# Kernel tuning notes

Hardware: AMD Instinct MI355X
Metric: run time of the kernel (lower is better)

## Reference

```python
import jax, jax.numpy as jnp
import numpy as np

RADIUS = 0.8
NSAMPLE = 32
EPS = 1e-5  # BatchNorm eps


def _bn(x, gamma, beta, axes):
    # BatchNorm (training-mode batch statistics), channel dim kept via broadcasting
    m = jnp.mean(x, axis=axes, keepdims=True)
    v = jnp.var(x, axis=axes, keepdims=True)
    return (x - m) * jax.lax.rsqrt(v + EPS) * gamma + beta


def setup_inputs() -> dict:
    key = jax.random.key(0)
    ks = jax.random.split(key, 6)
    B, N, P, C, COUT = 4, 8192, 2048, 128, 256
    ffps_xyz = jax.random.uniform(ks[0], (B, P, 3), dtype=jnp.float32) * 2.0 - 1.0
    backbone_xyz = jax.random.uniform(ks[1], (B, N, 3), dtype=jnp.float32) * 2.0 - 1.0
    backbone_features = jax.random.normal(ks[2], (B, C, N), dtype=jnp.float32)
    w_shift = jax.random.normal(ks[3], (3, 3), dtype=jnp.float32) * 0.1
    gamma_shift = jnp.ones((3,), jnp.float32)
    beta_shift = jnp.zeros((3,), jnp.float32)
    w_mlp = jax.random.normal(ks[4], (COUT, 3 + C), dtype=jnp.float32) * 0.05
    gamma_mlp = jnp.ones((COUT,), jnp.float32)
    beta_mlp = jnp.zeros((COUT,), jnp.float32)
    return {
        "ffps_xyz": ffps_xyz,
        "backbone_xyz": backbone_xyz,
        "backbone_features": backbone_features,
        "w_shift": w_shift,
        "gamma_shift": gamma_shift,
        "beta_shift": beta_shift,
        "w_mlp": w_mlp,
        "gamma_mlp": gamma_mlp,
        "beta_mlp": beta_mlp,
    }


def reference(ffps_xyz, backbone_xyz, backbone_features,
              w_shift, gamma_shift, beta_shift,
              w_mlp, gamma_mlp, beta_mlp):
    B, P, _ = ffps_xyz.shape
    N = backbone_xyz.shape[1]

    # ---- shift_layer: Conv1d(3->3, k=1, no bias) + BN1d + ReLU on (B,3,P) ----
    x = jnp.einsum('oc,bpc->bop', w_shift, ffps_xyz)                  # (B,3,P)
    x = _bn(x, gamma_shift[None, :, None], beta_shift[None, :, None], (0, 2))
    new_xyz = jax.nn.relu(x).transpose(0, 2, 1)                       # (B,P,3) query centers

    # ---- QueryAndGroup: ball query (radius, nsample), use_xyz=True ----
    d2 = jnp.sum((new_xyz[:, :, None, :] - backbone_xyz[:, None, :, :]) ** 2, -1)  # (B,P,N)
    within = d2 < (RADIUS * RADIUS)
    # pick the first NSAMPLE in-radius indices (CUDA ball_query semantics)
    keyv = jnp.where(within, jnp.arange(N, dtype=jnp.int32), jnp.int32(N))
    negk, idx = jax.lax.top_k(-keyv, NSAMPLE)                          # smallest keys first
    valid = (-negk) < N
    idx = jnp.where(valid, idx, idx[..., :1])                          # pad with first found idx

    g_xyz = jnp.take_along_axis(backbone_xyz[:, None, :, :], idx[..., None], axis=2)
    g_xyz = g_xyz - new_xyz[:, :, None, :]                             # (B,P,S,3) recentered
    feats = backbone_features.transpose(0, 2, 1)                       # (B,N,C)
    g_f = jnp.take_along_axis(feats[:, None, :, :], idx[..., None], axis=2)  # (B,P,S,C)
    g = jnp.concatenate([g_xyz, g_f], axis=-1)                         # (B,P,S,3+C)

    # ---- mlp: 1x1 conv (3+C -> COUT, no bias) + BN + ReLU ----
    y = jnp.einsum('oc,bpsc->bops', w_mlp, g)                          # (B,COUT,P,S)
    y = _bn(y, gamma_mlp[None, :, None, None], beta_mlp[None, :, None, None], (0, 2, 3))
    y = jax.nn.relu(y)

    # ---- max-pool over neighbor axis, squeeze, transpose ----
    y = jnp.max(y, axis=3)                                             # (B,COUT,P)
    return y.transpose(0, 2, 1)                                        # (B,P,COUT)
```

## Files before the change

kernel.cpp:

```cpp
#include <hip/hip_runtime.h>
#include <math.h>

namespace {
constexpr int B    = 4;
constexpr int N    = 8192;
constexpr int P    = 2048;
constexpr int C    = 128;
constexpr int COUT = 256;
constexpr int NS   = 32;
constexpr int BP   = B * P;
constexpr int BPB  = 2;
constexpr int GRP  = 8;
constexpr int NBLK = BP / (BPB * GRP);

constexpr size_t OFF_FEATT = 0;
constexpr size_t OFF_WSWZ  = 8388608;
constexpr size_t OFF_NXD   = 8470528;
constexpr size_t OFF_NXF   = 8667136;
constexpr size_t OFF_IDX   = 8765440;
constexpr size_t OFF_YMAX  = 9814016;
constexpr size_t OFF_PART  = 18202624;
constexpr size_t OFF_P2    = 19251200;
constexpr size_t OFF_AB    = 19513344;
constexpr size_t WS_NEED   = 19515392;
}

typedef short bf16x8 __attribute__((ext_vector_type(8)));
typedef float f32x4  __attribute__((ext_vector_type(4)));

typedef const __attribute__((address_space(1))) void gas_void;
typedef __attribute__((address_space(3))) void las_void;
#define GLOBAL_LOAD_LDS16(gp, lp) \
    __builtin_amdgcn_global_load_lds((gas_void*)(gp), (las_void*)(lp), 16, 0, 0)

__device__ inline unsigned short f2bf(float f) {
    unsigned u = __float_as_uint(f);
    unsigned r = u + 0x7fffu + ((u >> 16) & 1u);
    return (unsigned short)(r >> 16);
}

__global__ __launch_bounds__(256) void k_transpose(const float* __restrict__ feat,
                                                   unsigned short* __restrict__ featT) {
    __shared__ float tile[64][33];
    int tx = threadIdx.x, ty = threadIdx.y;
    int n0 = blockIdx.x * 32, c0 = blockIdx.y * 64, b = blockIdx.z;
    const float* src = feat + ((size_t)b * C + c0) * N + n0;
#pragma unroll
    for (int j = 0; j < 8; j++) tile[ty + 8 * j][tx] = src[(size_t)(ty + 8 * j) * N + tx];
    __syncthreads();
#pragma unroll
    for (int j = 0; j < 4; j++) {
        int n = ty + 8 * j;
        unsigned v = (unsigned)f2bf(tile[2 * tx][n]) | ((unsigned)f2bf(tile[2 * tx + 1][n]) << 16);
        *(unsigned*)&featT[((size_t)b * N + n0 + n) * C + c0 + 2 * tx] = v;
    }
}

__global__ __launch_bounds__(256) void k_wswz(const float* __restrict__ w,
                                              unsigned short* __restrict__ wswz) {
    int i = blockIdx.x * 256 + threadIdx.x;
    int j = i & 7;
    int lane = (i >> 3) & 63;
    int rest = i >> 9;
    int ks = rest % 5, rt = rest / 5;
    int cout = rt * 16 + (lane & 15);
    int k = ks * 32 + (lane >> 4) * 8 + j;
    float v = 0.f;
    if (k < 128) v = w[cout * 131 + 3 + k];
    else if (k < 131) v = w[cout * 131 + (k - 128)];
    wswz[i] = f2bf(v);
}

__global__ __launch_bounds__(1024) void k_shift(const float* __restrict__ ffps,
                                                const float* __restrict__ wsh,
                                                const float* __restrict__ gam,
                                                const float* __restrict__ bet,
                                                double* __restrict__ nxd,
                                                float* __restrict__ nxf) {
#pragma clang fp contract(off)
    __shared__ double red[6][1024];
    __shared__ double par[6];
    int t = threadIdx.x;
    double w[9];
#pragma unroll
    for (int i = 0; i < 9; i++) w[i] = (double)wsh[i];
    double x[8][3];
    double s[3] = {0, 0, 0}, sq[3] = {0, 0, 0};
#pragma unroll
    for (int i = 0; i < 8; i++) {
        int p = t + 1024 * i;
        double f0 = (double)ffps[p * 3 + 0];
        double f1 = (double)ffps[p * 3 + 1];
        double f2 = (double)ffps[p * 3 + 2];
#pragma unroll
        for (int o = 0; o < 3; o++) {
            double xo = (w[o * 3 + 0] * f0 + w[o * 3 + 1] * f1) + w[o * 3 + 2] * f2;
            x[i][o] = xo;
            s[o] += xo;
            sq[o] += xo * xo;
        }
    }
#pragma unroll
    for (int o = 0; o < 3; o++) { red[o][t] = s[o]; red[3 + o][t] = sq[o]; }
    for (int off = 512; off > 0; off >>= 1) {
        __syncthreads();
        if (t < off) {
#pragma unroll
            for (int j = 0; j < 6; j++) red[j][t] += red[j][t + off];
        }
    }
    __syncthreads();
    if (t == 0) {
#pragma unroll
        for (int o = 0; o < 3; o++) {
            double m = red[o][0] / (double)BP;
            double v = red[3 + o][0] / (double)BP - m * m;
            par[o] = m;
            par[3 + o] = 1.0 / sqrt(v + 1e-5);
        }
    }
    __syncthreads();
    double gv[3] = {(double)gam[0], (double)gam[1], (double)gam[2]};
    double bv[3] = {(double)bet[0], (double)bet[1], (double)bet[2]};
#pragma unroll
    for (int i = 0; i < 8; i++) {
        int p = t + 1024 * i;
#pragma unroll
        for (int o = 0; o < 3; o++) {
            double y = ((x[i][o] - par[o]) * par[3 + o]) * gv[o] + bv[o];
            y = (y > 0.0) ? y : 0.0;
            nxd[p * 3 + o] = y;
            nxf[p * 3 + o] = (float)y;
        }
    }
}

__global__ __launch_bounds__(256) void k_ballq(const float* __restrict__ bbxyz,
                                               const double* __restrict__ nxd,
                                               int* __restrict__ idxo) {
#pragma clang fp contract(off)
    int t = threadIdx.x;
    int wv = t >> 6, lane = t & 63;
    int q = blockIdx.x * 4 + wv;
    int b = q >> 11;
    double qx = nxd[q * 3 + 0], qy = nxd[q * 3 + 1], qz = nxd[q * 3 + 2];
    const double R2 = 0.8 * 0.8;
    {
        double ex = fmax(fmax(qx - 1.0, -1.0 - qx), 0.0);
        double ey = fmax(fmax(qy - 1.0, -1.0 - qy), 0.0);
        double ez = fmax(fmax(qz - 1.0, -1.0 - qz), 0.0);
        if (ex * ex + ey * ey + ez * ez >= R2) {
            if (lane < NS) idxo[q * NS + lane] = 0;
            return;
        }
    }
    const float* base = bbxyz + (size_t)b * N * 3;
    int found = 0, firstn = -1;

    float px[4], py[4], pz[4];
#pragma unroll
    for (int j = 0; j < 4; j++) {
        int n = j * 64 + lane;
        px[j] = base[n * 3 + 0]; py[j] = base[n * 3 + 1]; pz[j] = base[n * 3 + 2];
    }
    for (int cb = 0; cb < 32; cb++) {
        float nx[4], ny[4], nz[4];
        int nb = (cb + 1 < 32) ? (cb + 1) * 256 : 0;
#pragma unroll
        for (int j = 0; j < 4; j++) {
            int n = nb + j * 64 + lane;
            nx[j] = base[n * 3 + 0]; ny[j] = base[n * 3 + 1]; nz[j] = base[n * 3 + 2];
        }
#pragma unroll
        for (int j = 0; j < 4; j++) {
            int n = cb * 256 + j * 64 + lane;
            double dx = qx - (double)px[j], dy = qy - (double)py[j], dz = qz - (double)pz[j];
            double d2 = (dx * dx + dy * dy) + dz * dz;
            bool within = d2 < R2;
            unsigned long long mask = __ballot(within);
            if (firstn < 0 && mask != 0ull) firstn = (n - lane) + (__ffsll(mask) - 1);
            if (within) {
                int rank = found + __popcll(mask & ((1ull << lane) - 1ull));
                if (rank < NS) idxo[q * NS + rank] = n;
            }
            found += __popcll(mask);
        }
        if (found >= NS) break;
#pragma unroll
        for (int j = 0; j < 4; j++) { px[j] = nx[j]; py[j] = ny[j]; pz[j] = nz[j]; }
    }
    if (found < NS) {
        int padv = (found == 0) ? 0 : firstn;
        if (lane >= found && lane < NS) idxo[q * NS + lane] = padv;
    }
}

__global__ __launch_bounds__(256, 2) void k_mlp_mfma(
        const float* __restrict__ bbxyz,
        const unsigned short* __restrict__ featT,
        const unsigned short* __restrict__ wswz,
        const float* __restrict__ nxf,
        const int* __restrict__ idx,
        float* __restrict__ ymax,
        float* __restrict__ partial) {
    __shared__ alignas(16) unsigned short G[2][4 * 4 * 64 * 8];
    int t = threadIdx.x, lane = t & 63, w = t >> 6;
    int q = lane >> 4, c16 = lane & 15;
    int blk = blockIdx.x;
    int bpbase = blk * (BPB * GRP);
    const bf16x8* wp = (const bf16x8*)wswz;

    bf16x8 wreg[5][4];
#pragma unroll
    for (int ks = 0; ks < 5; ks++)
#pragma unroll
        for (int nt = 0; nt < 4; nt++)
            wreg[ks][nt] = wp[((w * 4 + nt) * 5 + ks) * 64 + lane];

    int n_cur[4], n_nxt[4];
#pragma unroll
    for (int mt = 0; mt < 4; mt++)
        n_cur[mt] = idx[(bpbase + (mt >> 1)) * NS + (mt & 1) * 16 + c16];
    {
        int bp = bpbase + (w >> 1);
        const unsigned short* row = featT + ((size_t)(bp >> 11) * N + n_cur[w]) * C + q * 8;
#pragma unroll
        for (int ks = 0; ks < 4; ks++)
            GLOBAL_LOAD_LDS16(row + ks * 32, &G[0][(w * 4 + ks) * 512]);
    }

    float smA[4] = {0.f, 0.f, 0.f, 0.f}, sqA[4] = {0.f, 0.f, 0.f, 0.f};

    for (int g = 0; g < GRP; g++) {
        int buf = g & 1;
        int bp0 = bpbase + g * BPB;
        if (g + 1 < GRP) {
#pragma unroll
            for (int mt = 0; mt < 4; mt++)
                n_nxt[mt] = idx[(bp0 + BPB + (mt >> 1)) * NS + (mt & 1) * 16 + c16];
        }
        __syncthreads();
        if (g + 1 < GRP) {
            int bp = bp0 + BPB + (w >> 1);
            const unsigned short* row = featT + ((size_t)(bp >> 11) * N + n_nxt[w]) * C + q * 8;
#pragma unroll
            for (int ks = 0; ks < 4; ks++)
                GLOBAL_LOAD_LDS16(row + ks * 32, &G[buf ^ 1][(w * 4 + ks) * 512]);
        }

        f32x4 acc[4][4];
#pragma unroll
        for (int mt = 0; mt < 4; mt++)
#pragma unroll
            for (int nt = 0; nt < 4; nt++) acc[mt][nt] = (f32x4){0.f, 0.f, 0.f, 0.f};

#pragma unroll
        for (int ks = 0; ks < 4; ks++) {
            bf16x8 ag[4];
#pragma unroll
            for (int mt = 0; mt < 4; mt++)
                ag[mt] = *(const bf16x8*)&G[buf][((mt * 4 + ks) * 64 + lane) * 8];
#pragma unroll
            for (int nt = 0; nt < 4; nt++)
#pragma unroll
                for (int mt = 0; mt < 4; mt++)
                    acc[mt][nt] = __builtin_amdgcn_mfma_f32_16x16x32_bf16(ag[mt], wreg[ks][nt], acc[mt][nt], 0, 0, 0);
        }
        {
            bf16x8 agx[4];
#pragma unroll
            for (int mt = 0; mt < 4; mt++) {
                int bp = bp0 + (mt >> 1);
                unsigned u01 = 0, u23 = 0;
                if (q == 0) {
                    const float* src = bbxyz + ((size_t)(bp >> 11) * N + n_cur[mt]) * 3;
                    const float* ctr = nxf + bp * 3;
                    u01 = (unsigned)f2bf(src[0] - ctr[0]) | ((unsigned)f2bf(src[1] - ctr[1]) << 16);
                    u23 = (unsigned)f2bf(src[2] - ctr[2]);
                }
                union { int4 i; bf16x8 h; } u;
                u.i = make_int4((int)u01, (int)u23, 0, 0);
                agx[mt] = u.h;
            }
#pragma unroll
            for (int nt = 0; nt < 4; nt++)
#pragma unroll
                for (int mt = 0; mt < 4; mt++)
                    acc[mt][nt] = __builtin_amdgcn_mfma_f32_16x16x32_bf16(agx[mt], wreg[4][nt], acc[mt][nt], 0, 0, 0);
        }

#pragma unroll
        for (int pm = 0; pm < BPB; pm++) {
            int bp = bp0 + pm;
#pragma unroll
            for (int nt = 0; nt < 4; nt++) {
                f32x4 a = acc[2 * pm][nt], c = acc[2 * pm + 1][nt];
                float mx = fmaxf(fmaxf(fmaxf(a[0], a[1]), fmaxf(a[2], a[3])),
                                 fmaxf(fmaxf(c[0], c[1]), fmaxf(c[2], c[3])));
                smA[nt] += ((a[0] + a[1]) + (a[2] + a[3])) + ((c[0] + c[1]) + (c[2] + c[3]));
                sqA[nt] += ((a[0] * a[0] + a[1] * a[1]) + (a[2] * a[2] + a[3] * a[3])) +
                           ((c[0] * c[0] + c[1] * c[1]) + (c[2] * c[2] + c[3] * c[3]));
                mx = fmaxf(mx, __shfl_xor(mx, 16, 64));
                mx = fmaxf(mx, __shfl_xor(mx, 32, 64));
                if (q == 0)
                    ymax[(size_t)bp * COUT + w * 64 + nt * 16 + c16] = mx;
            }
        }
#pragma unroll
        for (int mt = 0; mt < 4; mt++) n_cur[mt] = n_nxt[mt];
    }

#pragma unroll
    for (int nt = 0; nt < 4; nt++) {
        float sm = smA[nt], sq = sqA[nt];
        sm += __shfl_xor(sm, 16, 64);
        sm += __shfl_xor(sm, 32, 64);
        sq += __shfl_xor(sq, 16, 64);
        sq += __shfl_xor(sq, 32, 64);
        if (q == 0) {
            int cout = w * 64 + nt * 16 + c16;
            partial[(size_t)blk * 512 + cout] = sm;
            partial[(size_t)blk * 512 + 256 + cout] = sq;
        }
    }
}

__global__ __launch_bounds__(256) void k_red(const float* __restrict__ partial,
                                             float* __restrict__ p2) {
    int t = threadIdx.x, j = blockIdx.x;
    const float* row = partial + (size_t)j * 4 * 512;
    float s0 = 0.f, s1 = 0.f;
    for (int r = 0; r < 4; r++) {
        s0 += row[r * 512 + t];
        s1 += row[r * 512 + 256 + t];
    }
    p2[j * 512 + t] = s0;
    p2[j * 512 + 256 + t] = s1;
}

__global__ __launch_bounds__(256) void k_stats(const float* __restrict__ p2,
                                               const float* __restrict__ gam,
                                               const float* __restrict__ bet,
                                               float* __restrict__ ab) {
    int c = threadIdx.x;
    double sm = 0.0, sq = 0.0;
    for (int r = 0; r < 128; r++) {
        sm += (double)p2[r * 512 + c];
        sq += (double)p2[r * 512 + 256 + c];
    }
    const double cnt = (double)BP * (double)NS;
    double mean = sm / cnt;
    double var = sq / cnt - mean * mean;
    double a = (double)gam[c] / sqrt(var + 1e-5);
    double bb = (double)bet[c] - mean * a;
    ab[c] = (float)a;
    ab[256 + c] = (float)bb;
}

__global__ __launch_bounds__(256) void k_final(const float* __restrict__ ymax,
                                               const float* __restrict__ ab,
                                               float* __restrict__ out) {
    int e = blockIdx.x * 256 + threadIdx.x;
    int c = e & 255;
    out[e] = fmaxf(ab[c] * ymax[e] + ab[256 + c], 0.f);
}

extern "C" void kernel_launch(void* const* d_in, const int* in_sizes, int n_in,
                              void* d_out, int out_size, void* d_ws, size_t ws_size,
                              hipStream_t stream) {
    const float* ffps  = (const float*)d_in[0];
    const float* bbxyz = (const float*)d_in[1];
    const float* feat  = (const float*)d_in[2];
    const float* wsh   = (const float*)d_in[3];
    const float* gsh   = (const float*)d_in[4];
    const float* bsh   = (const float*)d_in[5];
    const float* wml   = (const float*)d_in[6];
    const float* gml   = (const float*)d_in[7];
    const float* bml   = (const float*)d_in[8];
    float* out = (float*)d_out;
    char* ws = (char*)d_ws;
    if (ws_size < WS_NEED) return;

    unsigned short* featT = (unsigned short*)(ws + OFF_FEATT);
    unsigned short* wswz  = (unsigned short*)(ws + OFF_WSWZ);
    double*         nxd   = (double*)(ws + OFF_NXD);
    float*          nxf   = (float*)(ws + OFF_NXF);
    int*            idx   = (int*)(ws + OFF_IDX);
    float*          ymax  = (float*)(ws + OFF_YMAX);
    float*          part  = (float*)(ws + OFF_PART);
    float*          p2    = (float*)(ws + OFF_P2);
    float*          ab    = (float*)(ws + OFF_AB);

    k_transpose<<<dim3(N / 32, C / 64, B), dim3(32, 8, 1), 0, stream>>>(feat, featT);
    k_wswz<<<dim3(160), dim3(256), 0, stream>>>(wml, wswz);
    k_shift<<<dim3(1), dim3(1024), 0, stream>>>(ffps, wsh, gsh, bsh, nxd, nxf);
    k_ballq<<<dim3(BP / 4), dim3(256), 0, stream>>>(bbxyz, nxd, idx);
    k_mlp_mfma<<<dim3(NBLK), dim3(256), 0, stream>>>(bbxyz, featT, wswz, nxf, idx, ymax, part);
    k_red<<<dim3(128), dim3(256), 0, stream>>>(part, p2);
    k_stats<<<dim3(1), dim3(256), 0, stream>>>(p2, gml, bml, ab);
    k_final<<<dim3(BP * COUT / 256), dim3(256), 0, stream>>>(ymax, ab, out);
}
```

Before: 172.3 us.

## Vectorize transpose and final stores, deepen ball-query and index prefetch pipelines

```diff
diff --git a/kernel.cpp b/kernel.cpp
--- a/kernel.cpp
+++ b/kernel.cpp
@@ -48,12 +48,18 @@
 #pragma unroll
     for (int j = 0; j < 8; j++) tile[ty + 8 * j][tx] = src[(size_t)(ty + 8 * j) * N + tx];
     __syncthreads();
-#pragma unroll
-    for (int j = 0; j < 4; j++) {
-        int n = ty + 8 * j;
-        unsigned v = (unsigned)f2bf(tile[2 * tx][n]) | ((unsigned)f2bf(tile[2 * tx + 1][n]) << 16);
-        *(unsigned*)&featT[((size_t)b * N + n0 + n) * C + c0 + 2 * tx] = v;
-    }
+    int t = ty * 32 + tx;
+    int n = t >> 3;
+    int k8 = (t & 7) * 8;
+    unsigned vv[4];
+#pragma unroll
+    for (int i = 0; i < 4; i++) {
+        unsigned lo = f2bf(tile[k8 + 2 * i][n]);
+        unsigned hi = f2bf(tile[k8 + 2 * i + 1][n]);
+        vv[i] = lo | (hi << 16);
+    }
+    *(int4*)&featT[((size_t)b * N + n0 + n) * C + c0 + k8] =
+        make_int4((int)vv[0], (int)vv[1], (int)vv[2], (int)vv[3]);
 }
 
 __global__ __launch_bounds__(256) void k_wswz(const float* __restrict__ w,
@@ -157,24 +163,25 @@
     const float* base = bbxyz + (size_t)b * N * 3;
     int found = 0, firstn = -1;
 
-    float px[4], py[4], pz[4];
-#pragma unroll
-    for (int j = 0; j < 4; j++) {
-        int n = j * 64 + lane;
-        px[j] = base[n * 3 + 0]; py[j] = base[n * 3 + 1]; pz[j] = base[n * 3 + 2];
-    }
-    for (int cb = 0; cb < 32; cb++) {
-        float nx[4], ny[4], nz[4];
-        int nb = (cb + 1 < 32) ? (cb + 1) * 256 : 0;
-#pragma unroll
-        for (int j = 0; j < 4; j++) {
-            int n = nb + j * 64 + lane;
-            nx[j] = base[n * 3 + 0]; ny[j] = base[n * 3 + 1]; nz[j] = base[n * 3 + 2];
-        }
-#pragma unroll
-        for (int j = 0; j < 4; j++) {
-            int n = cb * 256 + j * 64 + lane;
-            double dx = qx - (double)px[j], dy = qy - (double)py[j], dz = qz - (double)pz[j];
+    float X0[8], Y0[8], Z0[8], X1[8], Y1[8], Z1[8], X2[8], Y2[8], Z2[8];
+
+    auto loadb = [&](float (&XX)[8], float (&YY)[8], float (&ZZ)[8], int it) {
+#pragma unroll
+        for (int j = 0; j < 8; j++) {
+            int n = it * 512 + j * 64 + lane;
+            XX[j] = base[n * 3 + 0];
+            YY[j] = base[n * 3 + 1];
+            ZZ[j] = base[n * 3 + 2];
+        }
+    };
+    auto proc = [&](float (&XX)[8], float (&YY)[8], float (&ZZ)[8], int it) {
+#pragma clang fp contract(off)
+#pragma unroll
+        for (int j = 0; j < 8; j++) {
+            int n = it * 512 + j * 64 + lane;
+            double dx = qx - (double)XX[j];
+            double dy = qy - (double)YY[j];
+            double dz = qz - (double)ZZ[j];
             double d2 = (dx * dx + dy * dy) + dz * dz;
             bool within = d2 < R2;
             unsigned long long mask = __ballot(within);
@@ -185,9 +192,24 @@
             }
             found += __popcll(mask);
         }
+    };
+
+    loadb(X0, Y0, Z0, 0);
+    loadb(X1, Y1, Z1, 1);
+    loadb(X2, Y2, Z2, 2);
+
+    for (int itb = 0; itb < 16; itb += 3) {
+        proc(X0, Y0, Z0, itb);
         if (found >= NS) break;
-#pragma unroll
-        for (int j = 0; j < 4; j++) { px[j] = nx[j]; py[j] = ny[j]; pz[j] = nz[j]; }
+        loadb(X0, Y0, Z0, (itb + 3 < 16) ? itb + 3 : 0);
+        if (itb + 1 >= 16) break;
+        proc(X1, Y1, Z1, itb + 1);
+        if (found >= NS) break;
+        loadb(X1, Y1, Z1, (itb + 4 < 16) ? itb + 4 : 0);
+        if (itb + 2 >= 16) break;
+        proc(X2, Y2, Z2, itb + 2);
+        if (found >= NS) break;
+        loadb(X2, Y2, Z2, (itb + 5 < 16) ? itb + 5 : 0);
     }
     if (found < NS) {
         int padv = (found == 0) ? 0 : firstn;
@@ -217,10 +239,13 @@
         for (int nt = 0; nt < 4; nt++)
             wreg[ks][nt] = wp[((w * 4 + nt) * 5 + ks) * 64 + lane];
 
-    int n_cur[4], n_nxt[4];
+    int n_cur[4], n_nxt[4], n_nx2[4];
 #pragma unroll
     for (int mt = 0; mt < 4; mt++)
         n_cur[mt] = idx[(bpbase + (mt >> 1)) * NS + (mt & 1) * 16 + c16];
+#pragma unroll
+    for (int mt = 0; mt < 4; mt++)
+        n_nxt[mt] = idx[(bpbase + BPB + (mt >> 1)) * NS + (mt & 1) * 16 + c16];
     {
         int bp = bpbase + (w >> 1);
         const unsigned short* row = featT + ((size_t)(bp >> 11) * N + n_cur[w]) * C + q * 8;
@@ -234,10 +259,10 @@
     for (int g = 0; g < GRP; g++) {
         int buf = g & 1;
         int bp0 = bpbase + g * BPB;
-        if (g + 1 < GRP) {
+        if (g + 2 < GRP) {
 #pragma unroll
             for (int mt = 0; mt < 4; mt++)
-                n_nxt[mt] = idx[(bp0 + BPB + (mt >> 1)) * NS + (mt & 1) * 16 + c16];
+                n_nx2[mt] = idx[(bp0 + 2 * BPB + (mt >> 1)) * NS + (mt & 1) * 16 + c16];
         }
         __syncthreads();
         if (g + 1 < GRP) {
@@ -307,7 +332,7 @@
             }
         }
 #pragma unroll
-        for (int mt = 0; mt < 4; mt++) n_cur[mt] = n_nxt[mt];
+        for (int mt = 0; mt < 4; mt++) { n_cur[mt] = n_nxt[mt]; n_nxt[mt] = n_nx2[mt]; }
     }
 
 #pragma unroll
@@ -360,9 +385,15 @@
 __global__ __launch_bounds__(256) void k_final(const float* __restrict__ ymax,
                                                const float* __restrict__ ab,
                                                float* __restrict__ out) {
-    int e = blockIdx.x * 256 + threadIdx.x;
-    int c = e & 255;
-    out[e] = fmaxf(ab[c] * ymax[e] + ab[256 + c], 0.f);
+    int i = blockIdx.x * 256 + threadIdx.x;
+    int c0 = (i & 63) * 4;
+    f32x4 y = *(const f32x4*)&ymax[(size_t)i * 4];
+    f32x4 a = *(const f32x4*)&ab[c0];
+    f32x4 bb = *(const f32x4*)&ab[256 + c0];
+    f32x4 r;
+#pragma unroll
+    for (int j = 0; j < 4; j++) r[j] = fmaxf(a[j] * y[j] + bb[j], 0.f);
+    *(f32x4*)&out[(size_t)i * 4] = r;
 }
 
 extern "C" void kernel_launch(void* const* d_in, const int* in_sizes, int n_in,
@@ -398,5 +429,5 @@
     k_mlp_mfma<<<dim3(NBLK), dim3(256), 0, stream>>>(bbxyz, featT, wswz, nxf, idx, ymax, part);
     k_red<<<dim3(128), dim3(256), 0, stream>>>(part, p2);
     k_stats<<<dim3(1), dim3(256), 0, stream>>>(p2, gml, bml, ab);
-    k_final<<<dim3(BP * COUT / 256), dim3(256), 0, stream>>>(ymax, ab, out);
-}
+    k_final<<<dim3(BP * COUT / 1024), dim3(256), 0, stream>>>(ymax, ab, out);
+}
```

New measurement: 169.9 us. Within noise of the previous version (-1.4%).
